# Kernel optimization log

Hardware: AMD Instinct MI355X
Metric: run time of the kernel (lower is better)

The kernel has to match this reference:

```python
import jax, jax.numpy as jnp
import numpy as np

B, NQ, NK, D, H, DH = 4, 2048, 2048, 512, 8, 64  # inner_dim = H*DH = 512 = query_dim


def setup_inputs() -> dict:
    key = jax.random.key(0)
    ks = jax.random.split(key, 9)
    s = 0.02
    return {
        "init_query": jax.random.normal(ks[0], (B, NQ, D), dtype=jnp.float32),
        "embedding": jax.random.normal(ks[1], (B, NK, D), dtype=jnp.float32),
        "Wq": jax.random.normal(ks[2], (D, H * DH), dtype=jnp.float32) * s,
        "Wk": jax.random.normal(ks[3], (D, H * DH), dtype=jnp.float32) * s,
        "Wv": jax.random.normal(ks[4], (D, H * DH), dtype=jnp.float32) * s,
        "W0": jax.random.normal(ks[5], (H * DH, D), dtype=jnp.float32) * s,
        "b0": jnp.zeros((D,), dtype=jnp.float32),
        "W1": jax.random.normal(ks[6], (D, D), dtype=jnp.float32) * s,
        "b1": jnp.zeros((D,), dtype=jnp.float32),
    }


def reference(init_query, embedding, Wq, Wk, Wv, W0, b0, W1, b1):
    b, nq, _ = init_query.shape
    nk = embedding.shape[1]
    # project and split heads -> [b, h, n, dh]
    q = (init_query @ Wq).reshape(b, nq, H, DH).transpose(0, 2, 1, 3)
    k = (embedding @ Wk).reshape(b, nk, H, DH).transpose(0, 2, 1, 3)
    v = (embedding @ Wv).reshape(b, nk, H, DH).transpose(0, 2, 1, 3)
    # offset attention: alpha=1 (no 1/sqrt(d) scale)
    scores = jnp.einsum("bhqd,bhkd->bhqk", q, k)
    # softmax over the QUERY axis (torch dim=1 of [B*H, Nq, Nk]), then renormalize rows
    probs = jax.nn.softmax(scores, axis=2)
    probs = probs / (1e-12 + probs.sum(axis=-1, keepdims=True))
    out = jnp.einsum("bhqk,bhkd->bhqd", probs, v)
    out = out.transpose(0, 2, 1, 3).reshape(b, nq, H * DH)  # merge heads
    out = init_query - (out @ W0 + b0)  # offset residual
    out = out @ W1 + b1  # final projection (dropout p=0 -> identity)
    return out
```

## Files before the change

kernel.cpp:

```cpp
#include <hip/hip_runtime.h>
#include <math.h>

#define BATCH 4
#define NQ 2048
#define NKEY 2048
#define DMODEL 512
#define NH 8
#define DHEAD 64
#define BH (BATCH * NH)

typedef __attribute__((ext_vector_type(8))) short short8;
typedef __attribute__((ext_vector_type(4))) float f32x4;

#define MFMA16(a, b, c) __builtin_amdgcn_mfma_f32_16x16x32_bf16((a), (b), (c), 0, 0, 0)

static __device__ __forceinline__ unsigned short f2b(float f) {
    union { float f; unsigned u; } v; v.f = f;
    unsigned r = (v.u + 0x7fffu + ((v.u >> 16) & 1u)) >> 16;
    return (unsigned short)r;
}

__launch_bounds__(256) __global__
void cast_x(const float* __restrict__ a, const float* __restrict__ b,
            unsigned short* __restrict__ da, unsigned short* __restrict__ db) {
    const float* s = blockIdx.y ? b : a;
    unsigned short* d = blockIdx.y ? db : da;
    size_t i = ((size_t)blockIdx.x * 256 + threadIdx.x) * 4;
    float4 v = *(const float4*)(s + i);
    ushort4 o;
    o.x = f2b(v.x); o.y = f2b(v.y); o.z = f2b(v.z); o.w = f2b(v.w);
    *(ushort4*)(d + i) = o;
}

__launch_bounds__(256) __global__
void trans_w(const float* __restrict__ w0, const float* __restrict__ w1,
             const float* __restrict__ w2, const float* __restrict__ w3,
             const float* __restrict__ w4, unsigned short* __restrict__ dst) {
    const float* src = (blockIdx.z == 0) ? w0 : (blockIdx.z == 1) ? w1 :
                       (blockIdx.z == 2) ? w2 : (blockIdx.z == 3) ? w3 : w4;
    unsigned short* out = dst + (size_t)blockIdx.z * DMODEL * DMODEL;
    __shared__ float t[32][33];
    const int tx = threadIdx.x & 31, ty = threadIdx.x >> 5;
    const int k0 = blockIdx.x * 32, n0 = blockIdx.y * 32;
    #pragma unroll
    for (int j = 0; j < 4; ++j)
        t[ty + j * 8][tx] = src[(size_t)(k0 + ty + j * 8) * DMODEL + n0 + tx];
    __syncthreads();
    #pragma unroll
    for (int j = 0; j < 4; ++j)
        out[(size_t)(n0 + ty + j * 8) * DMODEL + k0 + tx] = f2b(t[tx][ty + j * 8]);
}

__device__ __forceinline__
void gemm_core(const unsigned short* __restrict__ A0,
               const unsigned short* __restrict__ B0,
               int K, int tid, unsigned short* Al, unsigned short* Bl,
               f32x4 acc[2][4]) {
    const int w = tid >> 6, lane = tid & 63;
    const int l16 = lane & 15, q4 = lane >> 4;
    char* AlB = (char*)Al;
    char* BlB = (char*)Bl;
    const int srow = tid >> 3;
    const int scolb = (tid & 7) * 16;
    const int skoff = (tid & 7) * 8;

    f32x4 z = {0.f, 0.f, 0.f, 0.f};
    #pragma unroll
    for (int i = 0; i < 2; ++i)
        #pragma unroll
        for (int t = 0; t < 4; ++t) acc[i][t] = z;

    short8 ast[4], bst[2];
    #pragma unroll
    for (int c = 0; c < 4; ++c)
        ast[c] = *(const short8*)(A0 + (size_t)(c * 32 + srow) * K + skoff);
    #pragma unroll
    for (int c = 0; c < 2; ++c)
        bst[c] = *(const short8*)(B0 + (size_t)(c * 32 + srow) * K + skoff);

    for (int k0 = 0; k0 < K; k0 += 64) {
        __syncthreads();
        #pragma unroll
        for (int c = 0; c < 4; ++c) {
            const int row = c * 32 + srow;
            *(short8*)(AlB + row * 128 + (scolb ^ ((row & 7) << 4))) = ast[c];
        }
        #pragma unroll
        for (int c = 0; c < 2; ++c) {
            const int row = c * 32 + srow;
            *(short8*)(BlB + row * 128 + (scolb ^ ((row & 7) << 4))) = bst[c];
        }
        if (k0 + 64 < K) {
            #pragma unroll
            for (int c = 0; c < 4; ++c)
                ast[c] = *(const short8*)(A0 + (size_t)(c * 32 + srow) * K + k0 + 64 + skoff);
            #pragma unroll
            for (int c = 0; c < 2; ++c)
                bst[c] = *(const short8*)(B0 + (size_t)(c * 32 + srow) * K + k0 + 64 + skoff);
        }
        __syncthreads();

        #pragma unroll
        for (int kk = 0; kk < 2; ++kk) {
            const int kb = kk * 64;
            const int rswA0 = ((w * 32 + l16) & 7) << 4;
            short8 a0 = *(const short8*)(AlB + (w * 32 + l16) * 128 + ((kb + q4 * 16) ^ rswA0));
            short8 a1 = *(const short8*)(AlB + (w * 32 + 16 + l16) * 128 + ((kb + q4 * 16) ^ rswA0));
            short8 bfr[4];
            #pragma unroll
            for (int t = 0; t < 4; ++t) {
                const int row = t * 16 + l16;
                bfr[t] = *(const short8*)(BlB + row * 128 + ((kb + q4 * 16) ^ ((row & 7) << 4)));
            }
            #pragma unroll
            for (int t = 0; t < 4; ++t) {
                acc[0][t] = MFMA16(a0, bfr[t], acc[0][t]);
                acc[1][t] = MFMA16(a1, bfr[t], acc[1][t]);
            }
        }
    }
}

__launch_bounds__(256) __global__
void gemm_qkv(const unsigned short* __restrict__ Xq,
              const unsigned short* __restrict__ Xe,
              const unsigned short* __restrict__ Wt,
              unsigned short* __restrict__ Qh,
              unsigned short* __restrict__ Kh,
              unsigned short* __restrict__ Vtb) {
    __shared__ unsigned short Al[128 * 64];
    __shared__ unsigned short Bl[64 * 64];
    const int tid = threadIdx.x;
    const int zsel = blockIdx.z;
    const int K = DMODEL;
    const unsigned short* A = (zsel == 0) ? Xq : Xe;
    const unsigned short* B0 = Wt + (size_t)zsel * DMODEL * DMODEL + (size_t)(blockIdx.y * 64) * K;
    const unsigned short* A0 = A + (size_t)(blockIdx.x * 128) * K;

    f32x4 acc[2][4];
    gemm_core(A0, B0, K, tid, Al, Bl, acc);

    const int w = tid >> 6, lane = tid & 63;
    const int l16 = lane & 15, q4 = lane >> 4;
    const int mBase = blockIdx.x * 128 + w * 32;
    const int n0 = blockIdx.y * 64;

    if (zsel < 2) {
        unsigned short* out = (zsel == 0) ? Qh : Kh;
        #pragma unroll
        for (int i = 0; i < 2; ++i)
            #pragma unroll
            for (int t = 0; t < 4; ++t)
                #pragma unroll
                for (int r = 0; r < 4; ++r) {
                    const int m = mBase + i * 16 + q4 * 4 + r;
                    const int n = n0 + t * 16 + l16;
                    out[(((size_t)(m >> 11) * NH + (n >> 6)) * NQ + (m & 2047)) * DHEAD + (n & 63)] = f2b(acc[i][t][r]);
                }
    } else {
        #pragma unroll
        for (int i = 0; i < 2; ++i)
            #pragma unroll
            for (int t = 0; t < 4; ++t) {
                const int m0 = mBase + i * 16 + q4 * 4;
                const int n = n0 + t * 16 + l16;
                ushort4 p;
                p.x = f2b(acc[i][t][0]); p.y = f2b(acc[i][t][1]);
                p.z = f2b(acc[i][t][2]); p.w = f2b(acc[i][t][3]);
                *(ushort4*)(Vtb + (((size_t)(m0 >> 11) * NH + (n >> 6)) * DHEAD + (n & 63)) * NKEY + (m0 & 2047)) = p;
            }
    }
}

template <int MODE>
__launch_bounds__(256) __global__
void gemm_bf16(const unsigned short* __restrict__ A,
               const unsigned short* __restrict__ Bt,
               void* __restrict__ Cout, const float* __restrict__ bias,
               const float* __restrict__ resid, int M, int N, int K) {
    __shared__ unsigned short Al[128 * 64];
    __shared__ unsigned short Bl[64 * 64];
    const int tid = threadIdx.x;
    const unsigned short* A0 = A + (size_t)(blockIdx.x * 128) * K;
    const unsigned short* B0 = Bt + (size_t)(blockIdx.y * 64) * K;

    f32x4 acc[2][4];
    gemm_core(A0, B0, K, tid, Al, Bl, acc);

    const int w = tid >> 6, lane = tid & 63;
    const int l16 = lane & 15, q4 = lane >> 4;
    const int mBase = blockIdx.x * 128 + w * 32;
    const int n0 = blockIdx.y * 64;

    #pragma unroll
    for (int i = 0; i < 2; ++i)
        #pragma unroll
        for (int t = 0; t < 4; ++t)
            #pragma unroll
            for (int r = 0; r < 4; ++r) {
                const int m = mBase + i * 16 + q4 * 4 + r;
                const int n = n0 + t * 16 + l16;
                float v = acc[i][t][r];
                if (MODE == 2) {
                    ((unsigned short*)Cout)[(size_t)m * N + n] = f2b(resid[(size_t)m * N + n] - (v + bias[n]));
                } else {
                    ((float*)Cout)[(size_t)m * N + n] = v + bias[n];
                }
            }
}

__launch_bounds__(256) __global__
void attn_pass1(const unsigned short* __restrict__ Qh,
                const unsigned short* __restrict__ Kh,
                float* __restrict__ colSrcp) {
    __shared__ unsigned short Qt[64 * 64];
    const int tid = threadIdx.x;
    const int w = tid >> 6, lane = tid & 63;
    const int l16 = lane & 15, q4 = lane >> 4;
    const int bh = blockIdx.y;
    const int kcol0 = blockIdx.x * 64 + w * 16;

    short8 bk0, bk1;
    {
        const unsigned short* Krow = Kh + ((size_t)bh * NKEY + kcol0 + l16) * DHEAD;
        bk0 = *(const short8*)(Krow + q4 * 8);
        bk1 = *(const short8*)(Krow + 32 + q4 * 8);
    }
    const unsigned short* Qb = Qh + (size_t)bh * NQ * DHEAD;
    char* QtB = (char*)Qt;
    const int srow = tid >> 3;
    const int scolb = (tid & 7) * 16;
    const int rsw = (l16 & 7) << 4;

    f32x4 z = {0.f, 0.f, 0.f, 0.f};
    float csum = 0.f;

    short8 qst[2];
    #pragma unroll
    for (int c = 0; c < 2; ++c)
        qst[c] = *(const short8*)(Qb + (size_t)(c * 32 + srow) * DHEAD + (scolb >> 1));

    for (int q0 = 0; q0 < NQ; q0 += 64) {
        __syncthreads();
        #pragma unroll
        for (int c = 0; c < 2; ++c) {
            const int row = c * 32 + srow;
            const int sw = scolb ^ ((row & 7) << 4);
            *(short8*)(QtB + row * 128 + sw) = qst[c];
        }
        if (q0 + 64 < NQ) {
            #pragma unroll
            for (int c = 0; c < 2; ++c)
                qst[c] = *(const short8*)(Qb + (size_t)(q0 + 64 + c * 32 + srow) * DHEAD + (scolb >> 1));
        }
        __syncthreads();
        #pragma unroll
        for (int qi = 0; qi < 4; ++qi) {
            const int row = qi * 16 + l16;
            short8 a0 = *(const short8*)(QtB + row * 128 + ((q4 * 16) ^ rsw));
            short8 a1 = *(const short8*)(QtB + row * 128 + ((64 + q4 * 16) ^ rsw));
            f32x4 s = MFMA16(a0, bk0, z);
            s = MFMA16(a1, bk1, s);
            csum += __expf(s[0]) + __expf(s[1]) + __expf(s[2]) + __expf(s[3]);
        }
    }
    csum += __shfl_xor(csum, 16, 64);
    csum += __shfl_xor(csum, 32, 64);
    if (q4 == 0)
        colSrcp[(size_t)bh * NKEY + kcol0 + l16] = 1.0f / csum;
}

__launch_bounds__(256) __global__
void attn_pass2(const unsigned short* __restrict__ Qh,
                const unsigned short* __restrict__ Kh,
                const unsigned short* __restrict__ Vt,
                const float* __restrict__ colSrcp,
                unsigned short* __restrict__ attnb) {
    __shared__ unsigned short Kt[64 * 64];
    __shared__ unsigned short Vtile[64 * 64];
    __shared__ unsigned short Elds[4][2][16][40];
    const int tid = threadIdx.x;
    const int w = tid >> 6, lane = tid & 63;
    const int l16 = lane & 15, q4 = lane >> 4;
    const int bh = blockIdx.y;
    const int b = bh >> 3, h = bh & 7;
    const int q0w = blockIdx.x * 64 + w * 16;

    short8 aq0, aq1;
    {
        const unsigned short* Qrow = Qh + ((size_t)bh * NQ + q0w + l16) * DHEAD;
        aq0 = *(const short8*)(Qrow + q4 * 8);
        aq1 = *(const short8*)(Qrow + 32 + q4 * 8);
    }
    const unsigned short* Kb = Kh + (size_t)bh * NKEY * DHEAD;
    const unsigned short* Vb = Vt + (size_t)bh * DHEAD * NKEY;
    const float* cs = colSrcp + (size_t)bh * NKEY;
    unsigned short* Ew = &Elds[w][0][0][0];
    char* KtB = (char*)Kt;
    char* VtB = (char*)Vtile;

    const int srow = tid >> 3;
    const int scolb = (tid & 7) * 16;
    const int rsw = (l16 & 7) << 4;

    f32x4 z = {0.f, 0.f, 0.f, 0.f};
    f32x4 o[4];
    #pragma unroll
    for (int t = 0; t < 4; ++t) o[t] = z;
    float rq[4] = {};

    short8 kst[2], vst[2];
    #pragma unroll
    for (int c = 0; c < 2; ++c) {
        const int row = c * 32 + srow;
        kst[c] = *(const short8*)(Kb + (size_t)row * DHEAD + (scolb >> 1));
        vst[c] = *(const short8*)(Vb + (size_t)row * NKEY + (scolb >> 1));
    }

    for (int k0 = 0; k0 < NKEY; k0 += 64) {
        __syncthreads();
        #pragma unroll
        for (int c = 0; c < 2; ++c) {
            const int row = c * 32 + srow;
            const int sw = scolb ^ ((row & 7) << 4);
            *(short8*)(KtB + row * 128 + sw) = kst[c];
            *(short8*)(VtB + row * 128 + sw) = vst[c];
        }
        if (k0 + 64 < NKEY) {
            #pragma unroll
            for (int c = 0; c < 2; ++c) {
                const int row = c * 32 + srow;
                kst[c] = *(const short8*)(Kb + (size_t)(k0 + 64 + row) * DHEAD + (scolb >> 1));
                vst[c] = *(const short8*)(Vb + (size_t)row * NKEY + (k0 + 64) + (scolb >> 1));
            }
        }
        float rcp[2][2];
        #pragma unroll
        for (int sub = 0; sub < 2; ++sub)
            #pragma unroll
            for (int j = 0; j < 2; ++j)
                rcp[sub][j] = cs[k0 + sub * 32 + j * 16 + l16];
        __syncthreads();

        #pragma unroll
        for (int sub = 0; sub < 2; ++sub) {
            short8 bk[2][2];
            #pragma unroll
            for (int j = 0; j < 2; ++j) {
                const int row = sub * 32 + j * 16 + l16;
                bk[j][0] = *(const short8*)(KtB + row * 128 + ((q4 * 16) ^ rsw));
                bk[j][1] = *(const short8*)(KtB + row * 128 + ((64 + q4 * 16) ^ rsw));
            }
            short8 bv[4];
            #pragma unroll
            for (int t = 0; t < 4; ++t) {
                const int row = t * 16 + l16;
                bv[t] = *(const short8*)(VtB + row * 128 + ((sub * 64 + q4 * 16) ^ rsw));
            }
            unsigned short* Eb = Ew + sub * (16 * 40);
            #pragma unroll
            for (int j = 0; j < 2; ++j) {
                f32x4 s = MFMA16(aq0, bk[j][0], z);
                s = MFMA16(aq1, bk[j][1], s);
                #pragma unroll
                for (int r = 0; r < 4; ++r) {
                    float e = __expf(s[r]) * rcp[sub][j];
                    rq[r] += e;
                    Eb[(q4 * 4 + r) * 40 + j * 16 + l16] = f2b(e);
                }
            }
            short8 ea = *(const short8*)(Eb + l16 * 40 + q4 * 8);
            #pragma unroll
            for (int t = 0; t < 4; ++t)
                o[t] = MFMA16(ea, bv[t], o[t]);
        }
    }

    #pragma unroll
    for (int r = 0; r < 4; ++r) {
        float v = rq[r];
        v += __shfl_xor(v, 1, 64);
        v += __shfl_xor(v, 2, 64);
        v += __shfl_xor(v, 4, 64);
        v += __shfl_xor(v, 8, 64);
        rq[r] = 1.0f / (1e-12f + v);
    }
    #pragma unroll
    for (int t = 0; t < 4; ++t)
        #pragma unroll
        for (int r = 0; r < 4; ++r) {
            const int q = q0w + q4 * 4 + r;
            attnb[((size_t)b * NQ + q) * DMODEL + h * DHEAD + t * 16 + l16] =
                f2b(o[t][r] * rq[r]);
        }
}

extern "C" void kernel_launch(void* const* d_in, const int* in_sizes, int n_in,
                              void* d_out, int out_size, void* d_ws, size_t ws_size,
                              hipStream_t stream) {
    const float* init_query = (const float*)d_in[0];
    const float* embedding  = (const float*)d_in[1];
    const float* Wq = (const float*)d_in[2];
    const float* Wk = (const float*)d_in[3];
    const float* Wv = (const float*)d_in[4];
    const float* W0 = (const float*)d_in[5];
    const float* b0 = (const float*)d_in[6];
    const float* W1 = (const float*)d_in[7];
    const float* b1 = (const float*)d_in[8];
    float* out = (float*)d_out;

    const size_t ACT = (size_t)BATCH * NQ * DMODEL;
    const size_t WEL = (size_t)DMODEL * DMODEL;

    unsigned short* Xq   = (unsigned short*)d_ws;
    unsigned short* Xe   = Xq + ACT;
    unsigned short* Wt   = Xe + ACT;
    unsigned short* Qh   = Wt + 5 * WEL;
    unsigned short* Kh   = Qh + ACT;
    unsigned short* Vtb  = Kh + ACT;
    unsigned short* attnb= Vtb + ACT;
    unsigned short* ybuf = attnb + ACT;
    float* colSrcp = (float*)(ybuf + ACT);

    unsigned short* W0t = Wt + 3 * WEL;
    unsigned short* W1t = Wt + 4 * WEL;

    const int M = BATCH * NQ;
    dim3 blk(256);
    dim3 gGemm(M / 128, DMODEL / 64);

    cast_x<<<dim3(ACT / 1024, 2), blk, 0, stream>>>(init_query, embedding, Xq, Xe);
    trans_w<<<dim3(16, 16, 5), blk, 0, stream>>>(Wq, Wk, Wv, W0, W1, Wt);

    gemm_qkv<<<dim3(M / 128, DMODEL / 64, 3), blk, 0, stream>>>(Xq, Xe, Wt, Qh, Kh, Vtb);

    attn_pass1<<<dim3(NKEY / 64, BH), blk, 0, stream>>>(Qh, Kh, colSrcp);
    attn_pass2<<<dim3(NQ / 64, BH), blk, 0, stream>>>(Qh, Kh, Vtb, colSrcp, attnb);

    gemm_bf16<2><<<gGemm, blk, 0, stream>>>(attnb, W0t, ybuf, b0, init_query, M, DMODEL, DMODEL);
    gemm_bf16<3><<<gGemm, blk, 0, stream>>>(ybuf, W1t, out, b1, nullptr, M, DMODEL, DMODEL);
}
```

Before: 244.6 us.

## Double-buffer attention LDS tiles and widen blocks to 512 threads

Both attention passes now use 512-thread blocks (8 waves) covering 128 keys or queries per block, so each staged Q, K or V tile is shared by twice as many waves. LDS tiles are double-buffered, so the next tile is written into the other buffer while the current one is consumed, leaving one barrier per iteration instead of two. Each thread loads one short8 per tile instead of two. In exchange the grid has half as many blocks (512 per pass), and LDS use and block size go up, which may lower occupancy.

```diff
diff --git a/kernel.cpp b/kernel.cpp
--- a/kernel.cpp
+++ b/kernel.cpp
@@ -209,16 +209,16 @@
             }
 }
 
-__launch_bounds__(256) __global__
+__launch_bounds__(512) __global__
 void attn_pass1(const unsigned short* __restrict__ Qh,
                 const unsigned short* __restrict__ Kh,
                 float* __restrict__ colSrcp) {
-    __shared__ unsigned short Qt[64 * 64];
+    __shared__ unsigned short Qt[2][64 * 64];
     const int tid = threadIdx.x;
     const int w = tid >> 6, lane = tid & 63;
     const int l16 = lane & 15, q4 = lane >> 4;
     const int bh = blockIdx.y;
-    const int kcol0 = blockIdx.x * 64 + w * 16;
+    const int kcol0 = blockIdx.x * 128 + w * 16;
 
     short8 bk0, bk1;
     {
@@ -227,33 +227,30 @@
         bk1 = *(const short8*)(Krow + 32 + q4 * 8);
     }
     const unsigned short* Qb = Qh + (size_t)bh * NQ * DHEAD;
-    char* QtB = (char*)Qt;
     const int srow = tid >> 3;
-    const int scolb = (tid & 7) * 16;
+    const int skoff = (tid & 7) * 8;
+    const int ssw = ((tid & 7) * 16) ^ ((srow & 7) << 4);
     const int rsw = (l16 & 7) << 4;
 
     f32x4 z = {0.f, 0.f, 0.f, 0.f};
     float csum = 0.f;
 
-    short8 qst[2];
-    #pragma unroll
-    for (int c = 0; c < 2; ++c)
-        qst[c] = *(const short8*)(Qb + (size_t)(c * 32 + srow) * DHEAD + (scolb >> 1));
-
-    for (int q0 = 0; q0 < NQ; q0 += 64) {
-        __syncthreads();
-        #pragma unroll
-        for (int c = 0; c < 2; ++c) {
-            const int row = c * 32 + srow;
-            const int sw = scolb ^ ((row & 7) << 4);
-            *(short8*)(QtB + row * 128 + sw) = qst[c];
-        }
-        if (q0 + 64 < NQ) {
-            #pragma unroll
-            for (int c = 0; c < 2; ++c)
-                qst[c] = *(const short8*)(Qb + (size_t)(q0 + 64 + c * 32 + srow) * DHEAD + (scolb >> 1));
-        }
-        __syncthreads();
+    short8 qst = *(const short8*)(Qb + (size_t)srow * DHEAD + skoff);
+    *(short8*)((char*)Qt[0] + srow * 128 + ssw) = qst;
+    qst = *(const short8*)(Qb + (size_t)(64 + srow) * DHEAD + skoff);
+    __syncthreads();
+
+    for (int it = 0; it < 32; ++it) {
+        const int q0 = it * 64;
+        char* QtB = (char*)Qt[it & 1];
+        char* QtN = (char*)Qt[(it & 1) ^ 1];
+
+        if (it < 31) {
+            *(short8*)(QtN + srow * 128 + ssw) = qst;
+            if (it < 30)
+                qst = *(const short8*)(Qb + (size_t)(q0 + 128 + srow) * DHEAD + skoff);
+        }
+
         #pragma unroll
         for (int qi = 0; qi < 4; ++qi) {
             const int row = qi * 16 + l16;
@@ -263,6 +260,7 @@
             s = MFMA16(a1, bk1, s);
             csum += __expf(s[0]) + __expf(s[1]) + __expf(s[2]) + __expf(s[3]);
         }
+        __syncthreads();
     }
     csum += __shfl_xor(csum, 16, 64);
     csum += __shfl_xor(csum, 32, 64);
@@ -270,21 +268,21 @@
         colSrcp[(size_t)bh * NKEY + kcol0 + l16] = 1.0f / csum;
 }
 
-__launch_bounds__(256) __global__
+__launch_bounds__(512) __global__
 void attn_pass2(const unsigned short* __restrict__ Qh,
                 const unsigned short* __restrict__ Kh,
                 const unsigned short* __restrict__ Vt,
                 const float* __restrict__ colSrcp,
                 unsigned short* __restrict__ attnb) {
-    __shared__ unsigned short Kt[64 * 64];
-    __shared__ unsigned short Vtile[64 * 64];
-    __shared__ unsigned short Elds[4][2][16][40];
+    __shared__ unsigned short Kt[2][64 * 64];
+    __shared__ unsigned short Vtile[2][64 * 64];
+    __shared__ unsigned short Elds[8][2][16][40];
     const int tid = threadIdx.x;
     const int w = tid >> 6, lane = tid & 63;
     const int l16 = lane & 15, q4 = lane >> 4;
     const int bh = blockIdx.y;
     const int b = bh >> 3, h = bh & 7;
-    const int q0w = blockIdx.x * 64 + w * 16;
+    const int q0w = blockIdx.x * 128 + w * 16;
 
     short8 aq0, aq1;
     {
@@ -296,11 +294,10 @@
     const unsigned short* Vb = Vt + (size_t)bh * DHEAD * NKEY;
     const float* cs = colSrcp + (size_t)bh * NKEY;
     unsigned short* Ew = &Elds[w][0][0][0];
-    char* KtB = (char*)Kt;
-    char* VtB = (char*)Vtile;
 
     const int srow = tid >> 3;
-    const int scolb = (tid & 7) * 16;
+    const int skoff = (tid & 7) * 8;
+    const int ssw = ((tid & 7) * 16) ^ ((srow & 7) << 4);
     const int rsw = (l16 & 7) << 4;
 
     f32x4 z = {0.f, 0.f, 0.f, 0.f};
@@ -309,38 +306,36 @@
     for (int t = 0; t < 4; ++t) o[t] = z;
     float rq[4] = {};
 
-    short8 kst[2], vst[2];
-    #pragma unroll
-    for (int c = 0; c < 2; ++c) {
-        const int row = c * 32 + srow;
-        kst[c] = *(const short8*)(Kb + (size_t)row * DHEAD + (scolb >> 1));
-        vst[c] = *(const short8*)(Vb + (size_t)row * NKEY + (scolb >> 1));
-    }
-
-    for (int k0 = 0; k0 < NKEY; k0 += 64) {
-        __syncthreads();
-        #pragma unroll
-        for (int c = 0; c < 2; ++c) {
-            const int row = c * 32 + srow;
-            const int sw = scolb ^ ((row & 7) << 4);
-            *(short8*)(KtB + row * 128 + sw) = kst[c];
-            *(short8*)(VtB + row * 128 + sw) = vst[c];
-        }
-        if (k0 + 64 < NKEY) {
-            #pragma unroll
-            for (int c = 0; c < 2; ++c) {
-                const int row = c * 32 + srow;
-                kst[c] = *(const short8*)(Kb + (size_t)(k0 + 64 + row) * DHEAD + (scolb >> 1));
-                vst[c] = *(const short8*)(Vb + (size_t)row * NKEY + (k0 + 64) + (scolb >> 1));
-            }
-        }
+    short8 kst = *(const short8*)(Kb + (size_t)srow * DHEAD + skoff);
+    short8 vst = *(const short8*)(Vb + (size_t)srow * NKEY + skoff);
+    *(short8*)((char*)Kt[0] + srow * 128 + ssw) = kst;
+    *(short8*)((char*)Vtile[0] + srow * 128 + ssw) = vst;
+    kst = *(const short8*)(Kb + (size_t)(64 + srow) * DHEAD + skoff);
+    vst = *(const short8*)(Vb + (size_t)srow * NKEY + 64 + skoff);
+    __syncthreads();
+
+    for (int it = 0; it < 32; ++it) {
+        const int k0 = it * 64;
+        char* KtB = (char*)Kt[it & 1];
+        char* VtB = (char*)Vtile[it & 1];
+        char* KtN = (char*)Kt[(it & 1) ^ 1];
+        char* VtN = (char*)Vtile[(it & 1) ^ 1];
+
         float rcp[2][2];
         #pragma unroll
         for (int sub = 0; sub < 2; ++sub)
             #pragma unroll
             for (int j = 0; j < 2; ++j)
                 rcp[sub][j] = cs[k0 + sub * 32 + j * 16 + l16];
-        __syncthreads();
+
+        if (it < 31) {
+            *(short8*)(KtN + srow * 128 + ssw) = kst;
+            *(short8*)(VtN + srow * 128 + ssw) = vst;
+            if (it < 30) {
+                kst = *(const short8*)(Kb + (size_t)(k0 + 128 + srow) * DHEAD + skoff);
+                vst = *(const short8*)(Vb + (size_t)srow * NKEY + (k0 + 128) + skoff);
+            }
+        }
 
         #pragma unroll
         for (int sub = 0; sub < 2; ++sub) {
@@ -374,6 +369,7 @@
             for (int t = 0; t < 4; ++t)
                 o[t] = MFMA16(ea, bv[t], o[t]);
         }
+        __syncthreads();
     }
 
     #pragma unroll
@@ -427,6 +423,7 @@
 
     const int M = BATCH * NQ;
     dim3 blk(256);
+    dim3 blk512(512);
     dim3 gGemm(M / 128, DMODEL / 64);
 
     cast_x<<<dim3(ACT / 1024, 2), blk, 0, stream>>>(init_query, embedding, Xq, Xe);
@@ -434,8 +431,8 @@
 
     gemm_qkv<<<dim3(M / 128, DMODEL / 64, 3), blk, 0, stream>>>(Xq, Xe, Wt, Qh, Kh, Vtb);
 
-    attn_pass1<<<dim3(NKEY / 64, BH), blk, 0, stream>>>(Qh, Kh, colSrcp);
-    attn_pass2<<<dim3(NQ / 64, BH), blk, 0, stream>>>(Qh, Kh, Vtb, colSrcp, attnb);
+    attn_pass1<<<dim3(NKEY / 128, BH), blk512, 0, stream>>>(Qh, Kh, colSrcp);
+    attn_pass2<<<dim3(NQ / 128, BH), blk512, 0, stream>>>(Qh, Kh, Vtb, colSrcp, attnb);
 
     gemm_bf16<2><<<gGemm, blk, 0, stream>>>(attnb, W0t, ybuf, b0, init_query, M, DMODEL, DMODEL);
     gemm_bf16<3><<<gGemm, blk, 0, stream>>>(ybuf, W1t, out, b1, nullptr, M, DMODEL, DMODEL);
```

Result: faster. 227.1 us (-7.2%).
